# Kernel tuning notes

Hardware: AMD Instinct MI355X
Metric: run time of the kernel (lower is better)

The kernel has to match this reference:

```python
import jax, jax.numpy as jnp
import numpy as np

B, L, F, H, K = 2048, 256, 64, 32, 2  # batch, seq len, features, g_hidden, LocalHilDim

def _dense_init(key, fan_in, fan_out):
    return (jax.random.normal(key, (fan_in, fan_out), jnp.float32) / np.sqrt(fan_in).astype(np.float32))

def setup_inputs() -> dict:
    key = jax.random.key(0)
    ks = jax.random.split(key, 12)
    s = jax.random.randint(ks[0], (B, L), 0, K)
    g = jax.random.normal(ks[1], (B,), jnp.float32)
    return dict(
        s=s, g=g,
        W_emb=_dense_init(ks[2], K, F), b_emb=jnp.zeros((F,), jnp.float32),
        W_g1=_dense_init(ks[3], 1, H), b_g1=jnp.zeros((H,), jnp.float32),
        W_g2=_dense_init(ks[4], H, F), b_g2=jnp.zeros((F,), jnp.float32),
        W_gh=_dense_init(ks[5], 1, F), b_gh=jnp.zeros((F,), jnp.float32),
        W_gc=_dense_init(ks[6], 1, F), b_gc=jnp.zeros((F,), jnp.float32),
        Wi=_dense_init(ks[7], F, 4 * F),  # fused input->gates (flax LSTMCell ii/if/ig/io, no bias)
        Wh=_dense_init(ks[8], F, 4 * F),  # fused hidden->gates (hi/hf/hg/ho)
        b_lstm=jnp.zeros((4 * F,), jnp.float32),  # fused gate biases
        W_amp=_dense_init(ks[9], F, K), b_amp=jnp.zeros((K,), jnp.float32),
    )

def reference(s, g, W_emb, b_emb, W_g1, b_g1, W_g2, b_g2, W_gh, b_gh, W_gc, b_gc, Wi, Wh, b_lstm, W_amp, b_amp):
    logProbFactor = 1.0
    g_in = g[:, None]                                            # [B,1]
    g_vec = jnp.tanh(g_in @ W_g1 + b_g1) @ W_g2 + b_g2          # g_mlp -> [B,F]
    h0 = g_in @ W_gh + b_gh                                      # init_carry h [B,F]
    c0 = g_in @ W_gc + b_gc                                      # init_carry c [B,F]
    s_pad = jnp.pad(s, ((0, 0), (1, 0)))                         # [B,L+1], leading 0 token
    seqy = jax.nn.one_hot(s_pad, K, dtype=jnp.float32)           # [B,L+1,K]
    emb = seqy @ W_emb + b_emb + g_vec[:, None, :]               # [B,L+1,F]
    # precompute input-side gate projections once: [B,L+1,4F]
    x_proj = emb @ Wi + b_lstm

    def step(carry, xt):                                         # xt: [B,4F]
        h, c = carry
        z = xt + h @ Wh
        zi, zf, zg, zo = jnp.split(z, 4, axis=-1)
        c = jax.nn.sigmoid(zf) * c + jax.nn.sigmoid(zi) * jnp.tanh(zg)
        h = jax.nn.sigmoid(zo) * jnp.tanh(c)
        return (h, c), h

    _, ys = jax.lax.scan(step, (h0, c0), jnp.swapaxes(x_proj, 0, 1))  # ys: [L+1,B,F]
    y = jnp.swapaxes(ys, 0, 1)                                   # [B,L+1,F]
    logits = y[:, :-1, :] @ W_amp + b_amp                        # [B,L,K]
    logp = jax.nn.log_softmax(logits) * logProbFactor
    token_logp = jnp.take_along_axis(logp, s[..., None], axis=-1)[..., 0]  # [B,L]
    return token_logp.sum(axis=-1)                               # [B]
```

## Files before the change

kernel.cpp:

```cpp
#include <hip/hip_runtime.h>


typedef __attribute__((ext_vector_type(8))) short bf16x8;
typedef __attribute__((ext_vector_type(4))) float f32x4;

#define L2E 1.44269504088896340736f
#define LN2 0.69314718055994530942f

__device__ __forceinline__ short f2bf(float x) {
    unsigned u = __builtin_bit_cast(unsigned, x);
    unsigned r = (u + 0x7FFFu + ((u >> 16) & 1u)) >> 16;
    return (short)r;
}

__global__ __launch_bounds__(256) void lstm_kernel(
    const int* __restrict__ s, const float* __restrict__ g,
    const float* __restrict__ W_emb, const float* __restrict__ b_emb,
    const float* __restrict__ W_g1, const float* __restrict__ b_g1,
    const float* __restrict__ W_g2, const float* __restrict__ b_g2,
    const float* __restrict__ W_gh, const float* __restrict__ b_gh,
    const float* __restrict__ W_gc, const float* __restrict__ b_gc,
    const float* __restrict__ Wi, const float* __restrict__ Wh,
    const float* __restrict__ b_lstm, const float* __restrict__ W_amp,
    const float* __restrict__ b_amp, float* __restrict__ out)
{
    __shared__ float Bx[35 * 256];
    __shared__ unsigned char sp_l[260];
    __shared__ __align__(16) short Hb[2][320];
    __shared__ float red[4][4];

    const int tid = threadIdx.x;
    const int w   = tid >> 6;
    const int l   = tid & 63;
    const int n2  = l & 15;
    const int q   = l >> 4;
    const int wgb = blockIdx.x * 4;

    {
        const int n = tid;
        const float sc = (n >= 128 && n < 192) ? (-2.0f * L2E) : (-L2E);
        float acc[35];
        #pragma unroll
        for (int i = 0; i < 35; ++i) acc[i] = 0.f;
        for (int f = 0; f < 64; ++f) {
            float wi = Wi[f * 256 + n] * sc;
            #pragma unroll
            for (int k = 0; k < 32; ++k) acc[k] += W_g2[k * 64 + f] * wi;
            acc[32] += W_emb[f] * wi;
            acc[33] += W_emb[64 + f] * wi;
            acc[34] += (b_emb[f] + b_g2[f]) * wi;
        }
        acc[34] += b_lstm[n] * sc;
        #pragma unroll
        for (int i = 0; i < 35; ++i) Bx[i * 256 + n] = acc[i];
    }
    {
        unsigned v = 0;
        #pragma unroll
        for (int b = 0; b < 4; ++b)
            v |= (unsigned)(s[(wgb + b) * 256 + tid] & 1) << b;
        sp_l[tid + 1] = (unsigned char)v;
        if (tid == 0) sp_l[0] = 0;
    }
    __syncthreads();

    bf16x8 Bf[4][2];
    float  Dsel[4];
    f32x4  C0[4];
    {
        bf16x8 B2f[4];
        float c0add[4];
        #pragma unroll
        for (int gi = 0; gi < 4; ++gi) {
            const int n = gi * 64 + w * 16 + n2;
            const float scg = (gi == 2) ? (-2.0f * L2E) : (-L2E);
            #pragma unroll
            for (int kf = 0; kf < 2; ++kf)
                #pragma unroll
                for (int j = 0; j < 8; ++j)
                    Bf[gi][kf][j] = f2bf(Wh[(kf * 32 + q * 8 + j) * 256 + n] * scg);
            #pragma unroll
            for (int j = 0; j < 8; ++j)
                B2f[gi][j] = f2bf(Bx[(q * 8 + j) * 256 + n]);
            c0add[gi] = Bx[32 * 256 + n] + Bx[34 * 256 + n];
            Dsel[gi]  = Bx[33 * 256 + n] - Bx[32 * 256 + n];
        }
        const float g_a = g[wgb + ((l >> 2) & 3)];
        bf16x8 Atv;
        #pragma unroll
        for (int j = 0; j < 8; ++j) {
            int k = q * 8 + j;
            Atv[j] = f2bf(tanhf(g_a * W_g1[k] + b_g1[k]));
        }
        const f32x4 zero4 = {0.f, 0.f, 0.f, 0.f};
        #pragma unroll
        for (int gi = 0; gi < 4; ++gi) {
            C0[gi] = __builtin_amdgcn_mfma_f32_16x16x32_bf16(Atv, B2f[gi], zero4, 0, 0, 0);
            #pragma unroll
            for (int r = 0; r < 4; ++r) C0[gi][r] += c0add[gi];
        }
    }
    bf16x8 BLd0, BLd1;
    f32x4 CL0;
    {
        #pragma unroll
        for (int j = 0; j < 8; ++j) {
            int k = q * 8 + j;
            BLd0[j] = (n2 == 0) ? f2bf(W_amp[k * 2 + 1] - W_amp[k * 2]) : (short)0;
            BLd1[j] = (n2 == 0) ? f2bf(W_amp[(k + 32) * 2 + 1] - W_amp[(k + 32) * 2]) : (short)0;
        }
        float bd = (n2 == 0) ? (b_amp[1] - b_amp[0]) : 0.f;
        CL0[0] = bd; CL0[1] = bd; CL0[2] = bd; CL0[3] = bd;
    }

    const int fcol  = w * 16 + n2;
    const int haddr = q * 80 + fcol;
    float cst;
    {
        float gb = g[wgb + q];
        cst = gb * W_gc[fcol] + b_gc[fcol];
        Hb[0][haddr] = f2bf(gb * W_gh[fcol] + b_gh[fcol]);
    }
    __syncthreads();

    const int ra = ((l >> 2) & 3) * 80 + q * 8;
    float slp = 0.f;
    unsigned spt = 0;

    auto step = [&](int t, int rb, bool doGate) {
        bf16x8 a0 = *(const bf16x8*)&Hb[rb][ra];
        bf16x8 a1 = *(const bf16x8*)&Hb[rb][ra + 32];
        unsigned spt_n = sp_l[t + 1];
        const unsigned bit = (spt >> q) & 1u;
        const float f_lane = (float)bit;

        f32x4 acc[4];
        #pragma unroll
        for (int gi = 0; gi < 4; ++gi) {
            f32x4 a;
            #pragma unroll
            for (int r = 0; r < 4; ++r)
                a[r] = __builtin_fmaf(f_lane, Dsel[gi], C0[gi][r]);
            a = __builtin_amdgcn_mfma_f32_16x16x32_bf16(a1, Bf[gi][1], a, 0, 0, 0);
            acc[gi] = __builtin_amdgcn_mfma_f32_16x16x32_bf16(a0, Bf[gi][0], a, 0, 0, 0);
        }

        const bool rr = (t >= 1) && (w == (t & 3));
        float dL = 0.f;
        if (rr) {
            f32x4 aL = __builtin_amdgcn_mfma_f32_16x16x32_bf16(a1, BLd1, CL0, 0, 0, 0);
            aL = __builtin_amdgcn_mfma_f32_16x16x32_bf16(a0, BLd0, aL, 0, 0, 0);
            dL = aL[0];
        }

        if (doGate) {
            const float yi = acc[0][0], yf = acc[1][0], yg = acc[2][0], yo = acc[3][0];
            float si = __builtin_amdgcn_rcpf(1.0f + __builtin_amdgcn_exp2f(yi));
            float sf = __builtin_amdgcn_rcpf(1.0f + __builtin_amdgcn_exp2f(yf));
            float so = __builtin_amdgcn_rcpf(1.0f + __builtin_amdgcn_exp2f(yo));
            float tg = 2.0f * __builtin_amdgcn_rcpf(1.0f + __builtin_amdgcn_exp2f(yg)) - 1.0f;
            float c  = sf * cst + si * tg;
            cst = c;
            float th = 2.0f * __builtin_amdgcn_rcpf(1.0f + __builtin_amdgcn_exp2f(-2.0f * L2E * c)) - 1.0f;
            float h  = so * th;
            unsigned hv;
            asm("v_cvt_pk_bf16_f32 %0, %1, %2" : "=v"(hv) : "v"(h), "v"(h));
            Hb[1 - rb][haddr] = (short)hv;
        }
        spt = spt_n;
        __syncthreads();

        if (rr) {
            float x = bit ? -dL : dL;
            float e = __builtin_amdgcn_exp2f(L2E * x);
            slp -= LN2 * __builtin_amdgcn_logf(1.0f + e);
        }
    };

    for (int t2 = 0; t2 < 256; t2 += 2) {
        step(t2, 0, true);
        step(t2 + 1, 1, true);
    }
    step(256, 0, false);

    if (n2 == 0) red[w][q] = slp;
    __syncthreads();
    if (tid < 4)
        out[wgb + tid] = red[0][tid] + red[1][tid] + red[2][tid] + red[3][tid];
}

extern "C" void kernel_launch(void* const* d_in, const int* in_sizes, int n_in,
                              void* d_out, int out_size, void* d_ws, size_t ws_size,
                              hipStream_t stream) {
    (void)in_sizes; (void)n_in; (void)out_size; (void)d_ws; (void)ws_size;
    const int*   s      = (const int*)d_in[0];
    const float* g      = (const float*)d_in[1];
    const float* W_emb  = (const float*)d_in[2];
    const float* b_emb  = (const float*)d_in[3];
    const float* W_g1   = (const float*)d_in[4];
    const float* b_g1   = (const float*)d_in[5];
    const float* W_g2   = (const float*)d_in[6];
    const float* b_g2   = (const float*)d_in[7];
    const float* W_gh   = (const float*)d_in[8];
    const float* b_gh   = (const float*)d_in[9];
    const float* W_gc   = (const float*)d_in[10];
    const float* b_gc   = (const float*)d_in[11];
    const float* Wi     = (const float*)d_in[12];
    const float* Wh     = (const float*)d_in[13];
    const float* b_lstm = (const float*)d_in[14];
    const float* W_amp  = (const float*)d_in[15];
    const float* b_amp  = (const float*)d_in[16];
    float* out = (float*)d_out;

    lstm_kernel<<<512, 256, 0, stream>>>(s, g, W_emb, b_emb, W_g1, b_g1, W_g2, b_g2,
                                         W_gh, b_gh, W_gc, b_gc, Wi, Wh, b_lstm,
                                         W_amp, b_amp, out);
}
```

Before: 233.1 us.

## Map one batch element per wavefront to drop per-step block barriers

Each wavefront now owns a single batch row and computes all 256 gate columns itself, using 32 MFMAs per step with lane selection. This removes the __syncthreads that previously ran every timestep across four waves sharing a hidden-state buffer. Logit differences go to shared memory and the log-sigmoid reduction is deferred to the end. The cost is 4x more MFMA work per step, most of it discarded by the lane selection, plus much higher register use for 16x2 weight fragments. Blocks grow to 512 threads, and the initial projection is computed in scalar FP32.

Result: slower. 362.5 us (+55.5%).

```diff
diff --git a/kernel.cpp b/kernel.cpp
--- a/kernel.cpp
+++ b/kernel.cpp
@@ -13,7 +13,7 @@
     return (short)r;
 }
 
-__global__ __launch_bounds__(256) void lstm_kernel(
+__global__ __launch_bounds__(512, 2) void lstm_kernel(
     const int* __restrict__ s, const float* __restrict__ g,
     const float* __restrict__ W_emb, const float* __restrict__ b_emb,
     const float* __restrict__ W_g1, const float* __restrict__ b_g1,
@@ -26,17 +26,18 @@
 {
     __shared__ float Bx[35 * 256];
     __shared__ unsigned char sp_l[260];
-    __shared__ __align__(16) short Hb[2][320];
-    __shared__ float red[4][4];
+    __shared__ __align__(16) short Hl[8][2][64];
+    __shared__ __align__(16) float dLb[8][256];
 
     const int tid = threadIdx.x;
     const int w   = tid >> 6;
     const int l   = tid & 63;
     const int n2  = l & 15;
     const int q   = l >> 4;
-    const int wgb = blockIdx.x * 4;
-
-    {
+    const int wgb = blockIdx.x * 8;
+    const int bat = wgb + w;
+
+    if (tid < 256) {
         const int n = tid;
         const float sc = (n >= 128 && n < 192) ? (-2.0f * L2E) : (-L2E);
         float acc[35];
@@ -53,53 +54,46 @@
         acc[34] += b_lstm[n] * sc;
         #pragma unroll
         for (int i = 0; i < 35; ++i) Bx[i * 256 + n] = acc[i];
-    }
-    {
         unsigned v = 0;
         #pragma unroll
-        for (int b = 0; b < 4; ++b)
-            v |= (unsigned)(s[(wgb + b) * 256 + tid] & 1) << b;
-        sp_l[tid + 1] = (unsigned char)v;
-        if (tid == 0) sp_l[0] = 0;
+        for (int b = 0; b < 8; ++b)
+            v |= (unsigned)(s[(wgb + b) * 256 + n] & 1) << b;
+        sp_l[n + 1] = (unsigned char)v;
+        if (n == 0) sp_l[0] = 0;
     }
     __syncthreads();
 
-    bf16x8 Bf[4][2];
-    float  Dsel[4];
-    f32x4  C0[4];
-    {
-        bf16x8 B2f[4];
-        float c0add[4];
-        #pragma unroll
-        for (int gi = 0; gi < 4; ++gi) {
-            const int n = gi * 64 + w * 16 + n2;
-            const float scg = (gi == 2) ? (-2.0f * L2E) : (-L2E);
-            #pragma unroll
-            for (int kf = 0; kf < 2; ++kf)
-                #pragma unroll
-                for (int j = 0; j < 8; ++j)
-                    Bf[gi][kf][j] = f2bf(Wh[(kf * 32 + q * 8 + j) * 256 + n] * scg);
+    bf16x8 Bf[16][2];
+    #pragma unroll
+    for (int m = 0; m < 16; ++m) {
+        const int n = m * 16 + n2;
+        const float scg = (m >= 8 && m < 12) ? (-2.0f * L2E) : (-L2E);
+        #pragma unroll
+        for (int kf = 0; kf < 2; ++kf)
             #pragma unroll
             for (int j = 0; j < 8; ++j)
-                B2f[gi][j] = f2bf(Bx[(q * 8 + j) * 256 + n]);
-            c0add[gi] = Bx[32 * 256 + n] + Bx[34 * 256 + n];
-            Dsel[gi]  = Bx[33 * 256 + n] - Bx[32 * 256 + n];
-        }
-        const float g_a = g[wgb + ((l >> 2) & 3)];
-        bf16x8 Atv;
-        #pragma unroll
-        for (int j = 0; j < 8; ++j) {
-            int k = q * 8 + j;
-            Atv[j] = f2bf(tanhf(g_a * W_g1[k] + b_g1[k]));
-        }
-        const f32x4 zero4 = {0.f, 0.f, 0.f, 0.f};
-        #pragma unroll
-        for (int gi = 0; gi < 4; ++gi) {
-            C0[gi] = __builtin_amdgcn_mfma_f32_16x16x32_bf16(Atv, B2f[gi], zero4, 0, 0, 0);
+                Bf[m][kf][j] = f2bf(Wh[(kf * 32 + q * 8 + j) * 256 + n] * scg);
+    }
+
+    const float g_b = g[bat];
+    float y0[4], Ds[4];
+    {
+        float atv[32];
+        #pragma unroll
+        for (int k = 0; k < 32; ++k)
+            atv[k] = tanhf(g_b * W_g1[k] + b_g1[k]);
+        #pragma unroll
+        for (int gt = 0; gt < 4; ++gt) {
+            const int n = gt * 64 + l;
+            float a = Bx[32 * 256 + n] + Bx[34 * 256 + n];
             #pragma unroll
-            for (int r = 0; r < 4; ++r) C0[gi][r] += c0add[gi];
-        }
-    }
+            for (int k = 0; k < 32; ++k)
+                a += atv[k] * Bx[k * 256 + n];
+            y0[gt] = a;
+            Ds[gt] = Bx[33 * 256 + n] - Bx[32 * 256 + n];
+        }
+    }
+
     bf16x8 BLd0, BLd1;
     f32x4 CL0;
     {
@@ -113,80 +107,73 @@
         CL0[0] = bd; CL0[1] = bd; CL0[2] = bd; CL0[3] = bd;
     }
 
-    const int fcol  = w * 16 + n2;
-    const int haddr = q * 80 + fcol;
-    float cst;
-    {
-        float gb = g[wgb + q];
-        cst = gb * W_gc[fcol] + b_gc[fcol];
-        Hb[0][haddr] = f2bf(gb * W_gh[fcol] + b_gh[fcol]);
-    }
-    __syncthreads();
-
-    const int ra = ((l >> 2) & 3) * 80 + q * 8;
-    float slp = 0.f;
-    unsigned spt = 0;
-
-    auto step = [&](int t, int rb, bool doGate) {
-        bf16x8 a0 = *(const bf16x8*)&Hb[rb][ra];
-        bf16x8 a1 = *(const bf16x8*)&Hb[rb][ra + 32];
-        unsigned spt_n = sp_l[t + 1];
-        const unsigned bit = (spt >> q) & 1u;
-        const float f_lane = (float)bit;
-
-        f32x4 acc[4];
-        #pragma unroll
-        for (int gi = 0; gi < 4; ++gi) {
-            f32x4 a;
-            #pragma unroll
-            for (int r = 0; r < 4; ++r)
-                a[r] = __builtin_fmaf(f_lane, Dsel[gi], C0[gi][r]);
-            a = __builtin_amdgcn_mfma_f32_16x16x32_bf16(a1, Bf[gi][1], a, 0, 0, 0);
-            acc[gi] = __builtin_amdgcn_mfma_f32_16x16x32_bf16(a0, Bf[gi][0], a, 0, 0, 0);
-        }
-
-        const bool rr = (t >= 1) && (w == (t & 3));
-        float dL = 0.f;
-        if (rr) {
+    float cs = (-2.0f * L2E) * (g_b * W_gc[l] + b_gc[l]);
+    Hl[w][0][l] = f2bf(g_b * W_gh[l] + b_gh[l]);
+
+    const bool qb0 = (q & 1) != 0;
+    const bool qb1 = (q & 2) != 0;
+
+    auto step = [&](int t, int rb, bool doLogit) {
+        bf16x8 a0 = *(const bf16x8*)&Hl[w][rb][q * 8];
+        bf16x8 a1 = *(const bf16x8*)&Hl[w][rb][32 + q * 8];
+        const unsigned bit = ((unsigned)sp_l[t] >> w) & 1u;
+        const float fb = (float)bit;
+        const f32x4 z4 = {0.f, 0.f, 0.f, 0.f};
+
+        float y[4];
+        #pragma unroll
+        for (int gt = 0; gt < 4; ++gt) {
+            f32x4 c0 = __builtin_amdgcn_mfma_f32_16x16x32_bf16(a1, Bf[4 * gt + 0][1], z4, 0, 0, 0);
+            c0 = __builtin_amdgcn_mfma_f32_16x16x32_bf16(a0, Bf[4 * gt + 0][0], c0, 0, 0, 0);
+            f32x4 c1 = __builtin_amdgcn_mfma_f32_16x16x32_bf16(a1, Bf[4 * gt + 1][1], z4, 0, 0, 0);
+            c1 = __builtin_amdgcn_mfma_f32_16x16x32_bf16(a0, Bf[4 * gt + 1][0], c1, 0, 0, 0);
+            f32x4 c2 = __builtin_amdgcn_mfma_f32_16x16x32_bf16(a1, Bf[4 * gt + 2][1], z4, 0, 0, 0);
+            c2 = __builtin_amdgcn_mfma_f32_16x16x32_bf16(a0, Bf[4 * gt + 2][0], c2, 0, 0, 0);
+            f32x4 c3 = __builtin_amdgcn_mfma_f32_16x16x32_bf16(a1, Bf[4 * gt + 3][1], z4, 0, 0, 0);
+            c3 = __builtin_amdgcn_mfma_f32_16x16x32_bf16(a0, Bf[4 * gt + 3][0], c3, 0, 0, 0);
+            float s01 = qb0 ? c1[0] : c0[0];
+            float s23 = qb0 ? c3[0] : c2[0];
+            y[gt] = __builtin_fmaf(fb, Ds[gt], (qb1 ? s23 : s01) + y0[gt]);
+        }
+
+        if (doLogit) {
             f32x4 aL = __builtin_amdgcn_mfma_f32_16x16x32_bf16(a1, BLd1, CL0, 0, 0, 0);
             aL = __builtin_amdgcn_mfma_f32_16x16x32_bf16(a0, BLd0, aL, 0, 0, 0);
-            dL = aL[0];
-        }
-
-        if (doGate) {
-            const float yi = acc[0][0], yf = acc[1][0], yg = acc[2][0], yo = acc[3][0];
-            float si = __builtin_amdgcn_rcpf(1.0f + __builtin_amdgcn_exp2f(yi));
-            float sf = __builtin_amdgcn_rcpf(1.0f + __builtin_amdgcn_exp2f(yf));
-            float so = __builtin_amdgcn_rcpf(1.0f + __builtin_amdgcn_exp2f(yo));
-            float tg = 2.0f * __builtin_amdgcn_rcpf(1.0f + __builtin_amdgcn_exp2f(yg)) - 1.0f;
-            float c  = sf * cst + si * tg;
-            cst = c;
-            float th = 2.0f * __builtin_amdgcn_rcpf(1.0f + __builtin_amdgcn_exp2f(-2.0f * L2E * c)) - 1.0f;
-            float h  = so * th;
-            unsigned hv;
-            asm("v_cvt_pk_bf16_f32 %0, %1, %2" : "=v"(hv) : "v"(h), "v"(h));
-            Hb[1 - rb][haddr] = (short)hv;
-        }
-        spt = spt_n;
-        __syncthreads();
-
-        if (rr) {
-            float x = bit ? -dL : dL;
-            float e = __builtin_amdgcn_exp2f(L2E * x);
-            slp -= LN2 * __builtin_amdgcn_logf(1.0f + e);
-        }
+            float dL = bit ? -aL[0] : aL[0];
+            if (l == 0) dLb[w][t - 1] = dL;
+        }
+
+        float si = __builtin_amdgcn_rcpf(1.0f + __builtin_amdgcn_exp2f(y[0]));
+        float sf = __builtin_amdgcn_rcpf(1.0f + __builtin_amdgcn_exp2f(y[1]));
+        float rg = __builtin_amdgcn_rcpf(1.0f + __builtin_amdgcn_exp2f(y[2]));
+        float so = __builtin_amdgcn_rcpf(1.0f + __builtin_amdgcn_exp2f(y[3]));
+        float tgs = __builtin_fmaf(-4.0f * L2E, rg, 2.0f * L2E);
+        cs = __builtin_fmaf(sf, cs, si * tgs);
+        float r5 = __builtin_amdgcn_rcpf(1.0f + __builtin_amdgcn_exp2f(cs));
+        float th = __builtin_fmaf(2.0f, r5, -1.0f);
+        float h  = so * th;
+        unsigned hv;
+        asm("v_cvt_pk_bf16_f32 %0, %1, %2" : "=v"(hv) : "v"(h), "v"(h));
+        Hl[w][rb ^ 1][l] = (short)hv;
     };
 
-    for (int t2 = 0; t2 < 256; t2 += 2) {
-        step(t2, 0, true);
-        step(t2 + 1, 1, true);
-    }
-    step(256, 0, false);
-
-    if (n2 == 0) red[w][q] = slp;
-    __syncthreads();
-    if (tid < 4)
-        out[wgb + tid] = red[0][tid] + red[1][tid] + red[2][tid] + red[3][tid];
+    step(0, 0, false);
+    for (int t = 1; t < 256; t += 2) {
+        step(t, 1, true);
+        step(t + 1, 0, true);
+    }
+
+    float accs = 0.f;
+    {
+        f32x4 v = *(const f32x4*)&dLb[w][l * 4];
+        #pragma unroll
+        for (int r = 0; r < 4; ++r)
+            accs += __builtin_amdgcn_logf(1.0f + __builtin_amdgcn_exp2f(L2E * v[r]));
+    }
+    #pragma unroll
+    for (int off = 1; off < 64; off <<= 1)
+        accs += __shfl_xor(accs, off, 64);
+    if (l == 0) out[bat] = -LN2 * accs;
 }
 
 extern "C" void kernel_launch(void* const* d_in, const int* in_sizes, int n_in,
@@ -212,7 +199,7 @@
     const float* b_amp  = (const float*)d_in[16];
     float* out = (float*)d_out;
 
-    lstm_kernel<<<512, 256, 0, stream>>>(s, g, W_emb, b_emb, W_g1, b_g1, W_g2, b_g2,
+    lstm_kernel<<<256, 512, 0, stream>>>(s, g, W_emb, b_emb, W_g1, b_g1, W_g2, b_g2,
                                          W_gh, b_gh, W_gc, b_gc, Wi, Wh, b_lstm,
                                          W_amp, b_amp, out);
 }
```
